# Kernel tuning notes

Measured on AMD Instinct MI355X. Metric: run time of the kernel, lower is better.

The kernel has to match this reference:

```python
import jax, jax.numpy as jnp
import numpy as np

NS, NC = 4, 3
DIAG = 4.1  # 4 + mass (mass = 0.1)
LAT = (16, 16, 16, 16)  # T, Z, Y, X


def setup_inputs() -> dict:
    key = jax.random.key(0)
    ks = jax.random.split(key, 6)
    psi_shape = LAT + (NS, NC)
    K_shape = (4,) + LAT + (NS * NC, NS * NC)
    return {
        "psi_re": jax.random.normal(ks[0], psi_shape, dtype=jnp.float32),
        "psi_im": jax.random.normal(ks[1], psi_shape, dtype=jnp.float32),
        "K_fwd_re": jax.random.normal(ks[2], K_shape, dtype=jnp.float32),
        "K_fwd_im": jax.random.normal(ks[3], K_shape, dtype=jnp.float32),
        "K_bwd_re": jax.random.normal(ks[4], K_shape, dtype=jnp.float32),
        "K_bwd_im": jax.random.normal(ks[5], K_shape, dtype=jnp.float32),
    }


def reference(psi_re, psi_im, K_fwd_re, K_fwd_im, K_bwd_re, K_bwd_im):
    # Flatten spin-color: (T,Z,Y,X,ns,nc) -> (T,Z,Y,X,ns*nc)
    pr = psi_re.reshape(psi_re.shape[:-2] + (NS * NC,))
    pi = psi_im.reshape(psi_im.shape[:-2] + (NS * NC,))
    out_re = DIAG * pr
    out_im = DIAG * pi
    for mu in range(4):
        ldim = mu - 5  # T,Z,Y,X axes of pr (which has 5 dims)
        Kfr, Kfi = K_fwd_re[mu], K_fwd_im[mu]
        Kbr, Kbi = K_bwd_re[mu], K_bwd_im[mu]
        pf_re = jnp.roll(pr, -1, axis=ldim)
        pf_im = jnp.roll(pi, -1, axis=ldim)
        pb_re = jnp.roll(pr, 1, axis=ldim)
        pb_im = jnp.roll(pi, 1, axis=ldim)
        # Complex 12x12 matvec per site: (K_re + i K_im) @ (p_re + i p_im)
        cf_re = jnp.einsum('...ij,...j->...i', Kfr, pf_re) - jnp.einsum('...ij,...j->...i', Kfi, pf_im)
        cf_im = jnp.einsum('...ij,...j->...i', Kfr, pf_im) + jnp.einsum('...ij,...j->...i', Kfi, pf_re)
        cb_re = jnp.einsum('...ij,...j->...i', Kbr, pb_re) - jnp.einsum('...ij,...j->...i', Kbi, pb_im)
        cb_im = jnp.einsum('...ij,...j->...i', Kbr, pb_im) + jnp.einsum('...ij,...j->...i', Kbi, pb_re)
        out_re = out_re - 0.5 * (cf_re + cb_re)
        out_im = out_im - 0.5 * (cf_im + cb_im)
    out_re = out_re.reshape(out_re.shape[:-1] + (NS, NC))
    out_im = out_im.reshape(out_im.shape[:-1] + (NS, NC))
    return (out_re, out_im)
```

## Files before the change

### kernel.cpp

```cpp
#include <hip/hip_runtime.h>

#define VOL   (16 * 16 * 16 * 16)
#define NSC   12
#define DIAG  4.1f

#define CMADD(kr, ki, vr, vi)                                              \
    sr += kr.x * vr.x - ki.x * vi.x;  si += kr.x * vi.x + ki.x * vr.x;     \
    sr += kr.y * vr.y - ki.y * vi.y;  si += kr.y * vi.y + ki.y * vr.y;     \
    sr += kr.z * vr.z - ki.z * vi.z;  si += kr.z * vi.z + ki.z * vr.z;     \
    sr += kr.w * vr.w - ki.w * vi.w;  si += kr.w * vi.w + ki.w * vr.w;

__global__ __launch_bounds__(256) void dslash_kernel(
    const float* __restrict__ psi_re, const float* __restrict__ psi_im,
    const float* __restrict__ Kf_re,  const float* __restrict__ Kf_im,
    const float* __restrict__ Kb_re,  const float* __restrict__ Kb_im,
    float* __restrict__ out_re,       float* __restrict__ out_im)
{
    const int tid = blockIdx.x * blockDim.x + threadIdx.x;
    if (tid >= VOL * NSC) return;

    const int site = tid / NSC;
    const int i    = tid - site * NSC;

    const int x = site        & 15;
    const int y = (site >> 4) & 15;
    const int z = (site >> 8) & 15;
    const int t = (site >> 12) & 15;

    float acc_re = DIAG * psi_re[site * NSC + i];
    float acc_im = DIAG * psi_im[site * NSC + i];

    const int coords [4] = {t, z, y, x};
    const int strides[4] = {4096, 256, 16, 1};

    #pragma unroll
    for (int mu = 0; mu < 4; ++mu) {
        const int c    = coords[mu];
        const int st   = strides[mu];
        const int base = site - c * st;
        const int sf   = base + ((c + 1)  & 15) * st;
        const int sb   = base + ((c + 15) & 15) * st;

        const int koff = (mu * VOL + site) * 144 + i * 12;
        const float4* kfr = (const float4*)(Kf_re + koff);
        const float4* kfi = (const float4*)(Kf_im + koff);
        const float4* kbr = (const float4*)(Kb_re + koff);
        const float4* kbi = (const float4*)(Kb_im + koff);

        const float4* pfr = (const float4*)(psi_re + sf * NSC);
        const float4* pfi = (const float4*)(psi_im + sf * NSC);
        const float4* pbr = (const float4*)(psi_re + sb * NSC);
        const float4* pbi = (const float4*)(psi_im + sb * NSC);

        float sr = 0.f, si = 0.f;
        #pragma unroll
        for (int q = 0; q < 3; ++q) {
            const float4 a  = kfr[q], b  = kfi[q];
            const float4 vr = pfr[q], vi = pfi[q];
            CMADD(a, b, vr, vi);
            const float4 c4 = kbr[q], d4 = kbi[q];
            const float4 wr = pbr[q], wi = pbi[q];
            CMADD(c4, d4, wr, wi);
        }
        acc_re -= 0.5f * sr;
        acc_im -= 0.5f * si;
    }

    out_re[tid] = acc_re;
    out_im[tid] = acc_im;
}

extern "C" void kernel_launch(void* const* d_in, const int* in_sizes, int n_in,
                              void* d_out, int out_size, void* d_ws, size_t ws_size,
                              hipStream_t stream) {
    const float* psi_re = (const float*)d_in[0];
    const float* psi_im = (const float*)d_in[1];
    const float* Kf_re  = (const float*)d_in[2];
    const float* Kf_im  = (const float*)d_in[3];
    const float* Kb_re  = (const float*)d_in[4];
    const float* Kb_im  = (const float*)d_in[5];

    float* out_re = (float*)d_out;
    float* out_im = (float*)d_out + (size_t)VOL * NSC;

    const int total  = VOL * NSC;
    const int block  = 256;
    const int grid   = (total + block - 1) / block;

    dslash_kernel<<<grid, block, 0, stream>>>(psi_re, psi_im,
                                              Kf_re, Kf_im, Kb_re, Kb_im,
                                              out_re, out_im);
}
```

Before: 125.9 us.

## Stage per-site K matrices into LDS via direct global-to-LDS loads

Each block now handles 16 sites with 192 threads. For each direction it cooperatively copies the forward and backward K matrices for those sites into shared memory using global_load_lds, then reads them from LDS for the matvec. The goal is fully coalesced streaming of the dominant K traffic. In exchange it adds two barriers per direction, removes loop unrolling over mu, and uses about 36 KB of LDS per block, which may limit occupancy and overlap.

```diff
diff --git a/kernel.cpp b/kernel.cpp
--- a/kernel.cpp
+++ b/kernel.cpp
@@ -1,8 +1,11 @@
 #include <hip/hip_runtime.h>
 
-#define VOL   (16 * 16 * 16 * 16)
+#define VOL   65536
 #define NSC   12
 #define DIAG  4.1f
+#define SPB   16
+#define THREADS (SPB * NSC)
+#define MATF  (SPB * 144)
 
 #define CMADD(kr, ki, vr, vi)                                              \
     sr += kr.x * vr.x - ki.x * vi.x;  si += kr.x * vi.x + ki.x * vr.x;     \
@@ -10,42 +13,63 @@
     sr += kr.z * vr.z - ki.z * vi.z;  si += kr.z * vi.z + ki.z * vr.z;     \
     sr += kr.w * vr.w - ki.w * vi.w;  si += kr.w * vi.w + ki.w * vr.w;
 
-__global__ __launch_bounds__(256) void dslash_kernel(
+__device__ __forceinline__ void g2lds16(const float* g, float* l) {
+    __builtin_amdgcn_global_load_lds(
+        (const __attribute__((address_space(1))) unsigned int*)g,
+        (__attribute__((address_space(3))) unsigned int*)l,
+        16, 0, 0);
+}
+
+__global__ __launch_bounds__(THREADS) void dslash_kernel(
     const float* __restrict__ psi_re, const float* __restrict__ psi_im,
     const float* __restrict__ Kf_re,  const float* __restrict__ Kf_im,
     const float* __restrict__ Kb_re,  const float* __restrict__ Kb_im,
     float* __restrict__ out_re,       float* __restrict__ out_im)
 {
-    const int tid = blockIdx.x * blockDim.x + threadIdx.x;
-    if (tid >= VOL * NSC) return;
+    __shared__ float lds[4 * MATF];
 
-    const int site = tid / NSC;
-    const int i    = tid - site * NSC;
+    const int j  = threadIdx.x;
+    const int w  = j >> 6;
+    const int l  = j & 63;
+    const int site0 = blockIdx.x * SPB;
+    const int sl = j / NSC;
+    const int i  = j - sl * NSC;
+    const int site = site0 + sl;
 
     const int x = site        & 15;
     const int y = (site >> 4) & 15;
     const int z = (site >> 8) & 15;
     const int t = (site >> 12) & 15;
+    const int coords [4] = {t, z, y, x};
+    const int strides[4] = {4096, 256, 16, 1};
 
     float acc_re = DIAG * psi_re[site * NSC + i];
     float acc_im = DIAG * psi_im[site * NSC + i];
 
-    const int coords [4] = {t, z, y, x};
-    const int strides[4] = {4096, 256, 16, 1};
+    const float* __restrict__ Ks[4] = {Kf_re, Kf_im, Kb_re, Kb_im};
 
-    #pragma unroll
     for (int mu = 0; mu < 4; ++mu) {
-        const int c    = coords[mu];
-        const int st   = strides[mu];
-        const int base = site - c * st;
-        const int sf   = base + ((c + 1)  & 15) * st;
-        const int sb   = base + ((c + 15) & 15) * st;
+        const size_t gbase = ((size_t)mu * VOL + (size_t)site0) * 144;
+        #pragma unroll
+        for (int m = 0; m < 4; ++m) {
+            const float* src = Ks[m] + gbase;
+            #pragma unroll
+            for (int jj = 0; jj < 3; ++jj) {
+                const int c = jj * 3 + w;
+                g2lds16(src + c * 256 + l * 4, &lds[m * MATF + c * 256 + l * 4]);
+            }
+        }
+        __syncthreads();
 
-        const int koff = (mu * VOL + site) * 144 + i * 12;
-        const float4* kfr = (const float4*)(Kf_re + koff);
-        const float4* kfi = (const float4*)(Kf_im + koff);
-        const float4* kbr = (const float4*)(Kb_re + koff);
-        const float4* kbi = (const float4*)(Kb_im + koff);
+        const int cc = coords[mu], st = strides[mu];
+        const int base = site - cc * st;
+        const int sf = base + ((cc + 1)  & 15) * st;
+        const int sb = base + ((cc + 15) & 15) * st;
+
+        const float4* kfr = (const float4*)&lds[0 * MATF + j * 12];
+        const float4* kfi = (const float4*)&lds[1 * MATF + j * 12];
+        const float4* kbr = (const float4*)&lds[2 * MATF + j * 12];
+        const float4* kbi = (const float4*)&lds[3 * MATF + j * 12];
 
         const float4* pfr = (const float4*)(psi_re + sf * NSC);
         const float4* pfi = (const float4*)(psi_im + sf * NSC);
@@ -64,10 +88,11 @@
         }
         acc_re -= 0.5f * sr;
         acc_im -= 0.5f * si;
+        __syncthreads();
     }
 
-    out_re[tid] = acc_re;
-    out_im[tid] = acc_im;
+    out_re[site * NSC + i] = acc_re;
+    out_im[site * NSC + i] = acc_im;
 }
 
 extern "C" void kernel_launch(void* const* d_in, const int* in_sizes, int n_in,
@@ -83,11 +108,9 @@
     float* out_re = (float*)d_out;
     float* out_im = (float*)d_out + (size_t)VOL * NSC;
 
-    const int total  = VOL * NSC;
-    const int block  = 256;
-    const int grid   = (total + block - 1) / block;
+    const int grid = VOL / SPB;
 
-    dslash_kernel<<<grid, block, 0, stream>>>(psi_re, psi_im,
-                                              Kf_re, Kf_im, Kb_re, Kb_im,
-                                              out_re, out_im);
+    dslash_kernel<<<grid, THREADS, 0, stream>>>(psi_re, psi_im,
+                                                Kf_re, Kf_im, Kb_re, Kb_im,
+                                                out_re, out_im);
 }
```

Result: faster. 114.7 us (-8.9%).
